# Optimization experiments

Hardware: AMD Instinct MI355X
Metric: run time of the kernel (lower is better)

## Reference

```python
import jax, jax.numpy as jnp
import numpy as np

B, H, W, DIM = 8, 32, 32, 768
HEADS = 12
HD = DIM // HEADS  # 64


def setup_inputs() -> dict:
    key = jax.random.key(0)
    ks = jax.random.split(key, 7)
    s = 0.02  # init scale to keep logits in a sane range
    return {
        "x": jax.random.normal(ks[0], (B, H, W, DIM), jnp.float32),
        "qkv_w": jax.random.normal(ks[1], (3 * DIM, DIM), jnp.float32) * s,
        "qkv_b": jax.random.normal(ks[2], (3 * DIM,), jnp.float32) * s,
        "proj_w": jax.random.normal(ks[3], (DIM, DIM), jnp.float32) * s,
        "proj_b": jax.random.normal(ks[4], (DIM,), jnp.float32) * s,
        "rel_pos_h": jax.random.normal(ks[5], (2 * H - 1, HD), jnp.float32) * s,
        "rel_pos_w": jax.random.normal(ks[6], (2 * W - 1, HD), jnp.float32) * s,
    }


def reference(x, qkv_w, qkv_b, proj_w, proj_b, rel_pos_h, rel_pos_w):
    b, h, w, dim = x.shape
    n = h * w
    hd = dim // HEADS
    scale = hd ** -0.5

    xf = x.reshape(b, n, dim)
    qkv = xf @ qkv_w.T + qkv_b                       # (B, N, 3*dim)
    qkv = qkv.reshape(b, n, 3, HEADS, hd)
    qkv = jnp.transpose(qkv, (2, 0, 3, 1, 4)).reshape(3, b * HEADS, n, hd)
    q, k, v = qkv[0], qkv[1], qkv[2]                 # each (B*heads, N, hd)

    # decomposed rel-pos bias (q_size == k_size -> pure index lookup)
    coords_h = jnp.arange(h)[:, None] - jnp.arange(h)[None, :] + (h - 1)
    coords_w = jnp.arange(w)[:, None] - jnp.arange(w)[None, :] + (w - 1)
    Rh = rel_pos_h[coords_h]                         # (H, H, hd)
    Rw = rel_pos_w[coords_w]                         # (W, W, hd)
    r_q = q.reshape(b * HEADS, h, w, hd)
    rel_h = jnp.einsum('bhwc,hkc->bhwk', r_q, Rh)    # (B*heads, H, W, H)
    rel_w = jnp.einsum('bhwc,wkc->bhwk', r_q, Rw)    # (B*heads, H, W, W)
    bias = (rel_h[:, :, :, :, None] + rel_w[:, :, :, None, :]).reshape(b * HEADS, n, n)

    attn = (q * scale) @ jnp.swapaxes(k, -2, -1) + bias
    attn = jax.nn.softmax(attn, axis=-1)
    out = attn @ v                                   # (B*heads, N, hd)

    out = out.reshape(b, HEADS, n, hd)
    out = jnp.transpose(out, (0, 2, 1, 3)).reshape(b, n, dim)
    out = out @ proj_w.T + proj_b
    return out.reshape(b, h, w, dim)
```

## Files before the change

kernel.cpp:

```cpp
#include <hip/hip_runtime.h>

typedef unsigned short u16;
typedef __attribute__((ext_vector_type(8))) short bf16x8;
typedef __attribute__((ext_vector_type(4))) short s16x4;
typedef __attribute__((ext_vector_type(4))) float f32x4;

__device__ __forceinline__ float bf2f(u16 u) {
  union { unsigned int i; float f; } v; v.i = ((unsigned int)u) << 16; return v.f;
}
__device__ __forceinline__ u16 f2bf(float f) {
  union { float f; unsigned int i; } v; v.f = f;
  unsigned int r = v.i + 0x7fffu + ((v.i >> 16) & 1u);
  return (u16)(r >> 16);
}
__device__ __forceinline__ f32x4 MFMA(bf16x8 a, bf16x8 b, f32x4 c) {
  return __builtin_amdgcn_mfma_f32_16x16x32_bf16(a, b, c, 0, 0, 0);
}
__device__ __forceinline__ void cvt8(const float* p, uint4* dst) {
  float4 f0 = *(const float4*)(p);
  float4 f1 = *(const float4*)(p + 4);
  u16* t = (u16*)dst;
  t[0] = f2bf(f0.x); t[1] = f2bf(f0.y); t[2] = f2bf(f0.z); t[3] = f2bf(f0.w);
  t[4] = f2bf(f1.x); t[5] = f2bf(f1.y); t[6] = f2bf(f1.z); t[7] = f2bf(f1.w);
}
__device__ __forceinline__ void gld16(const u16* g, u16* l) {
  __builtin_amdgcn_global_load_lds(
      (const __attribute__((address_space(1))) unsigned int*)g,
      (__attribute__((address_space(3))) unsigned int*)l, 16, 0, 0);
}

#define N8_X  786432
#define N8_QW 221184
#define N8_PW 73728
__global__ __launch_bounds__(256) void cast_kernel(
    const float* __restrict__ x, const float* __restrict__ qw, const float* __restrict__ pw,
    u16* __restrict__ xb, u16* __restrict__ qwb, u16* __restrict__ pwb)
{
  const int i = blockIdx.x * 256 + threadIdx.x;
  const float* s; u16* d; int off;
  if (i < N8_X)            { s = x;  d = xb;  off = i; }
  else if (i < N8_X+N8_QW) { s = qw; d = qwb; off = i - N8_X; }
  else                     { s = pw; d = pwb; off = i - (N8_X + N8_QW); }
  uint4 pk; cvt8(s + (size_t)off * 8, &pk);
  *(uint4*)(d + (size_t)off * 8) = pk;
}

template<int MODE>
__global__ __launch_bounds__(256) void gemm_bt(
    const u16* __restrict__ A, const u16* __restrict__ Bw, const float* __restrict__ bias,
    void* __restrict__ C0v, u16* __restrict__ C1, u16* __restrict__ C2,
    int M, int N, int K)
{
  __shared__ u16 sA[128 * 32];
  __shared__ u16 sB[128 * 32];
  const int tid = threadIdx.x;
  const int lane = tid & 63, wv = tid >> 6;
  const int wr = wv >> 1, wc = wv & 1;
  const int l16 = lane & 15, quad = lane >> 4;
  const int m0 = blockIdx.y << 7, n0 = blockIdx.x << 7;

  const int srow = tid >> 2, scol = (tid & 3) << 3;
  const u16* gA0 = A  + (size_t)(m0 + srow) * K + scol;
  const u16* gB0 = Bw + (size_t)(n0 + srow) * K + scol;
  const u16* gA1 = gA0 + (size_t)64 * K;
  const u16* gB1 = gB0 + (size_t)64 * K;
  u16* const lwA0 = sA + wv * 512;
  u16* const lwA1 = sA + 2048 + wv * 512;
  u16* const lwB0 = sB + wv * 512;
  u16* const lwB1 = sB + 2048 + wv * 512;

  f32x4 acc[4][4];
  #pragma unroll
  for (int i = 0; i < 4; ++i)
    #pragma unroll
    for (int j = 0; j < 4; ++j) {
      acc[i][j][0] = 0.f; acc[i][j][1] = 0.f; acc[i][j][2] = 0.f; acc[i][j][3] = 0.f;
    }

  for (int k0 = 0; k0 < K; k0 += 32) {
    __syncthreads();
    gld16(gA0 + k0, lwA0);
    gld16(gA1 + k0, lwA1);
    gld16(gB0 + k0, lwB0);
    gld16(gB1 + k0, lwB1);
    __syncthreads();
    bf16x8 af[4], bfr[4];
    #pragma unroll
    for (int i = 0; i < 4; ++i)
      af[i] = *(const bf16x8*)(sA + (wr * 64 + i * 16 + l16) * 32 + quad * 8);
    #pragma unroll
    for (int j = 0; j < 4; ++j)
      bfr[j] = *(const bf16x8*)(sB + (wc * 64 + j * 16 + l16) * 32 + quad * 8);
    #pragma unroll
    for (int i = 0; i < 4; ++i)
      #pragma unroll
      for (int j = 0; j < 4; ++j)
        acc[i][j] = MFMA(af[i], bfr[j], acc[i][j]);
  }

  #pragma unroll
  for (int j = 0; j < 4; ++j) {
    const int n = n0 + wc * 64 + j * 16 + l16;
    const float bv = bias[n];
    if (MODE == 0) {
      float* C0 = (float*)C0v;
      #pragma unroll
      for (int i = 0; i < 4; ++i) {
        const int m = m0 + wr * 64 + i * 16 + quad * 4;
        #pragma unroll
        for (int r = 0; r < 4; ++r)
          C0[(size_t)(m + r) * N + n] = acc[i][j][r] + bv;
      }
    } else {
      u16* C0 = (u16*)C0v;
      const int which = n / 768;
      const int rem = n - which * 768;
      const int head = rem >> 6, c = rem & 63;
      #pragma unroll
      for (int i = 0; i < 4; ++i) {
        const int m = m0 + wr * 64 + i * 16 + quad * 4;
        const int b = m >> 10, npos = m & 1023;
        const size_t bh = (size_t)(b * 12 + head);
        if (which == 0) {
          #pragma unroll
          for (int r = 0; r < 4; ++r)
            C0[(bh << 16) + ((size_t)(npos + r) << 6) + c] = f2bf(acc[i][j][r] + bv);
        } else if (which == 1) {
          #pragma unroll
          for (int r = 0; r < 4; ++r)
            C1[(bh << 16) + ((size_t)(npos + r) << 6) + c] = f2bf(acc[i][j][r] + bv);
        } else {
          s16x4 pk;
          #pragma unroll
          for (int r = 0; r < 4; ++r) pk[r] = (short)f2bf(acc[i][j][r] + bv);
          *(s16x4*)(C2 + (bh << 16) + ((size_t)c << 10) + npos) = pk;
        }
      }
    }
  }
}

__global__ __launch_bounds__(256) void attn_kernel(
    const u16* __restrict__ Q, const u16* __restrict__ Kt, const u16* __restrict__ VT,
    const float* __restrict__ rph, const float* __restrict__ rpw,
    u16* __restrict__ Oa)
{
  __shared__ __align__(16) u16 uni[18432];
  __shared__ u16 sSh[4 * 32 * 36];
  __shared__ float sL[4][32];

  u16* const uRPH = uni;
  u16* const uRPW = uni + 4536;
  u16* const uSw  = uni;
  u16* const sK   = uni;
  u16* const sVT  = uni + 4608;
  u16* const sP   = uni + 9216;

  const int tid = threadIdx.x;
  const int wave = tid >> 6, lane = tid & 63;
  const int l16 = lane & 15, quad = lane >> 4;
  const int bh = blockIdx.x >> 3, qt = blockIdx.x & 7;
  const int qrow0 = (qt << 7) + (wave << 5);
  const int qh = qrow0 >> 5;

  bf16x8 qf[2][2];
  #pragma unroll
  for (int nq = 0; nq < 2; ++nq) {
    const u16* qp = Q + (((size_t)bh << 10) + qrow0 + nq * 16 + l16) * 64 + quad * 8;
    qf[nq][0] = *(const bf16x8*)(qp);
    qf[nq][1] = *(const bf16x8*)(qp + 32);
  }

  for (int j = tid; j < 64 * 8; j += 256) {
    const int row = j >> 3, ck = (j & 7) << 3;
    uint4 vw;
    if (row < 63) cvt8(rpw + (size_t)row * 64 + ck, &vw);
    else { vw.x = 0u; vw.y = 0u; vw.z = 0u; vw.w = 0u; }
    *(uint4*)(uRPW + row * 72 + ck) = vw;
    if (row < 63) {
      uint4 vh;
      cvt8(rph + (size_t)row * 64 + ck, &vh);
      *(uint4*)(uRPH + row * 72 + ck) = vh;
    }
  }
  __syncthreads();

  #pragma unroll
  for (int tk = 0; tk < 2; ++tk) {
    const int kh = tk * 16 + l16;
    const u16* bp = uRPH + (qh + 31 - kh) * 72 + quad * 8;
    bf16x8 b0 = *(const bf16x8*)(bp);
    bf16x8 b1 = *(const bf16x8*)(bp + 32);
    #pragma unroll
    for (int nq = 0; nq < 2; ++nq) {
      f32x4 c; c[0] = 0.f; c[1] = 0.f; c[2] = 0.f; c[3] = 0.f;
      c = MFMA(qf[nq][0], b0, c);
      c = MFMA(qf[nq][1], b1, c);
      #pragma unroll
      for (int r = 0; r < 4; ++r)
        sSh[wave * 1152 + (nq * 16 + quad * 4 + r) * 36 + tk * 16 + l16] = f2bf(c[r]);
    }
  }

  f32x4 swc[2][4];
  #pragma unroll
  for (int tj = 0; tj < 4; ++tj) {
    const u16* bp = uRPW + (tj * 16 + l16) * 72 + quad * 8;
    bf16x8 b0 = *(const bf16x8*)(bp);
    bf16x8 b1 = *(const bf16x8*)(bp + 32);
    #pragma unroll
    for (int nq = 0; nq < 2; ++nq) {
      f32x4 c; c[0] = 0.f; c[1] = 0.f; c[2] = 0.f; c[3] = 0.f;
      c = MFMA(qf[nq][0], b0, c);
      c = MFMA(qf[nq][1], b1, c);
      swc[nq][tj] = c;
    }
  }
  __syncthreads();

  #pragma unroll
  for (int tj = 0; tj < 4; ++tj)
    #pragma unroll
    for (int nq = 0; nq < 2; ++nq)
      #pragma unroll
      for (int r = 0; r < 4; ++r)
        uSw[wave * 2304 + (nq * 16 + quad * 4 + r) * 72 + tj * 16 + l16] =
            f2bf(swc[nq][tj][r]);

  float rw[2][2][4];
  #pragma unroll
  for (int nq = 0; nq < 2; ++nq) {
    const int q = nq * 16 + l16;
    #pragma unroll
    for (int hi = 0; hi < 2; ++hi)
      #pragma unroll
      for (int r = 0; r < 4; ++r) {
        const int kw = hi * 16 + quad * 4 + r;
        rw[nq][hi][r] = bf2f(uSw[wave * 2304 + q * 72 + (q - kw + 31)]);
      }
  }

  f32x4 oacc[2][4];
  #pragma unroll
  for (int nq = 0; nq < 2; ++nq)
    #pragma unroll
    for (int nd = 0; nd < 4; ++nd) {
      oacc[nq][nd][0] = 0.f; oacc[nq][nd][1] = 0.f; oacc[nq][nd][2] = 0.f; oacc[nq][nd][3] = 0.f;
    }
  float lsum[2] = {0.f, 0.f};

  for (int kt = 0; kt < 16; ++kt) {
    const int kb = kt << 6;
    uint4 kreg[2], vreg[2];
    #pragma unroll
    for (int t = 0; t < 2; ++t) {
      const int j = tid + (t << 8);
      const int row = j >> 3, ck = (j & 7) << 3;
      kreg[t] = *(const uint4*)(Kt + (((size_t)bh << 10) + kb + row) * 64 + ck);
      vreg[t] = *(const uint4*)(VT + (((size_t)bh << 6) + row) * 1024 + kb + ck);
    }
    float rh[2][2];
    #pragma unroll
    for (int nq = 0; nq < 2; ++nq) {
      const unsigned int w2 =
          *(const unsigned int*)(sSh + wave * 1152 + (nq * 16 + l16) * 36 + (kt << 1));
      rh[nq][0] = bf2f((u16)(w2 & 0xffffu));
      rh[nq][1] = bf2f((u16)(w2 >> 16));
    }
    __syncthreads();
    #pragma unroll
    for (int t = 0; t < 2; ++t) {
      const int j = tid + (t << 8);
      const int row = j >> 3, ck = (j & 7) << 3;
      *(uint4*)(sK + row * 72 + ck) = kreg[t];
      *(uint4*)(sVT + row * 72 + ck) = vreg[t];
    }
    __syncthreads();

    f32x4 sacc[4][2];
    #pragma unroll
    for (int mk = 0; mk < 4; ++mk) {
      const u16* kp = sK + (mk * 16 + l16) * 72 + quad * 8;
      bf16x8 kf0 = *(const bf16x8*)(kp);
      bf16x8 kf1 = *(const bf16x8*)(kp + 32);
      #pragma unroll
      for (int nq = 0; nq < 2; ++nq) {
        f32x4 t4; t4[0] = 0.f; t4[1] = 0.f; t4[2] = 0.f; t4[3] = 0.f;
        t4 = MFMA(kf0, qf[nq][0], t4);
        t4 = MFMA(kf1, qf[nq][1], t4);
        sacc[mk][nq] = t4;
      }
    }
    #pragma unroll
    for (int nq = 0; nq < 2; ++nq) {
      #pragma unroll
      for (int mk = 0; mk < 4; ++mk) {
        const float rhv = rh[nq][mk >> 1];
        s16x4 pk;
        #pragma unroll
        for (int r = 0; r < 4; ++r) {
          const float s = sacc[mk][nq][r] * 0.125f + rhv + rw[nq][mk & 1][r];
          const float p = __expf(s);
          lsum[nq] += p;
          pk[r] = (short)f2bf(p);
        }
        *(s16x4*)(&sP[(wave << 11) + (wave << 8) + (nq * 16 + l16) * 72 + mk * 16 + quad * 4]) = pk;
      }
    }
    const u16* pw = sP + (wave << 11) + (wave << 8);
    #pragma unroll
    for (int ks = 0; ks < 2; ++ks) {
      bf16x8 ap0 = *(const bf16x8*)(pw + (l16) * 72 + ks * 32 + quad * 8);
      bf16x8 ap1 = *(const bf16x8*)(pw + (16 + l16) * 72 + ks * 32 + quad * 8);
      #pragma unroll
      for (int nd = 0; nd < 4; ++nd) {
        bf16x8 bv = *(const bf16x8*)(sVT + (nd * 16 + l16) * 72 + ks * 32 + quad * 8);
        oacc[0][nd] = MFMA(ap0, bv, oacc[0][nd]);
        oacc[1][nd] = MFMA(ap1, bv, oacc[1][nd]);
      }
    }
  }

  #pragma unroll
  for (int nq = 0; nq < 2; ++nq) {
    lsum[nq] += __shfl_xor(lsum[nq], 16);
    lsum[nq] += __shfl_xor(lsum[nq], 32);
  }
  if (lane < 16) { sL[wave][l16] = lsum[0]; sL[wave][16 + l16] = lsum[1]; }

  const int b = bh / 12, head = bh - b * 12;
  #pragma unroll
  for (int nq = 0; nq < 2; ++nq) {
    #pragma unroll
    for (int r = 0; r < 4; ++r) {
      const int ql = nq * 16 + quad * 4 + r;
      const float linv = 1.0f / sL[wave][ql];
      const size_t base = ((size_t)(b << 10) + qrow0 + ql) * 768 + head * 64 + l16;
      #pragma unroll
      for (int nd = 0; nd < 4; ++nd)
        Oa[base + nd * 16] = f2bf(oacc[nq][nd][r] * linv);
    }
  }
}

extern "C" void kernel_launch(void* const* d_in, const int* in_sizes, int n_in,
                              void* d_out, int out_size, void* d_ws, size_t ws_size,
                              hipStream_t stream) {
  (void)in_sizes; (void)n_in; (void)out_size; (void)ws_size;
  const float* x      = (const float*)d_in[0];
  const float* qkv_w  = (const float*)d_in[1];
  const float* qkv_b  = (const float*)d_in[2];
  const float* proj_w = (const float*)d_in[3];
  const float* proj_b = (const float*)d_in[4];
  const float* rph    = (const float*)d_in[5];
  const float* rpw    = (const float*)d_in[6];
  float* out = (float*)d_out;

  char* ws = (char*)d_ws;
  const size_t SZ = (size_t)96 * 1024 * 64;
  u16* Qw  = (u16*)ws;
  u16* Kw  = Qw + SZ;
  u16* VTw = Kw + SZ;
  u16* Xb  = VTw + SZ;
  u16* Oa  = Xb;
  u16* QWb = Xb + SZ;
  u16* PWb = QWb + (size_t)2304 * 768;

  cast_kernel<<<4224, 256, 0, stream>>>(x, qkv_w, proj_w, Xb, QWb, PWb);
  gemm_bt<1><<<dim3(18, 64), 256, 0, stream>>>(Xb, QWb, qkv_b, Qw, Kw, VTw, 8192, 2304, 768);
  attn_kernel<<<768, 256, 0, stream>>>(Qw, Kw, VTw, rph, rpw, Oa);
  gemm_bt<0><<<dim3(6, 64), 256, 0, stream>>>(Oa, PWb, proj_b, out, nullptr, nullptr, 8192, 768, 768);
}
```

Baseline: 251.1 us.

## Prefetch K/V tiles, remap block order, and vectorize attention output stores

The attention kernel now issues the global loads for the next K/V tile right after the shared-memory store barrier, so they overlap with the current tile's MFMA work instead of stalling at the top of each iteration. The PV MFMA operands are swapped so each lane holds four contiguous output columns, which lets the row sum stay in registers (the shared-memory sL exchange is gone) and the output be written as 8-byte vector stores. Both GEMMs and the attention kernel switch to a 1D grid with a remapped block order that groups 8 M-tiles (or 8 heads) per chunk, aiming for better L2/MALL reuse of shared operands. The cost is more live registers for the prefetch, plus one redundant reload on the last iteration.

Measured after the change: 283.5 us. 12.9% more time.

```diff
diff --git a/kernel.cpp b/kernel.cpp
--- a/kernel.cpp
+++ b/kernel.cpp
@@ -45,7 +45,7 @@
   *(uint4*)(d + (size_t)off * 8) = pk;
 }
 
-template<int MODE>
+template<int MODE, int NXB>
 __global__ __launch_bounds__(256) void gemm_bt(
     const u16* __restrict__ A, const u16* __restrict__ Bw, const float* __restrict__ bias,
     void* __restrict__ C0v, u16* __restrict__ C1, u16* __restrict__ C2,
@@ -57,7 +57,11 @@
   const int lane = tid & 63, wv = tid >> 6;
   const int wr = wv >> 1, wc = wv & 1;
   const int l16 = lane & 15, quad = lane >> 4;
-  const int m0 = blockIdx.y << 7, n0 = blockIdx.x << 7;
+  const int bi = blockIdx.x;
+  const int t = bi >> 3;
+  const int nx = t % NXB;
+  const int my = ((t / NXB) << 3) | (bi & 7);
+  const int m0 = my << 7, n0 = nx << 7;
 
   const int srow = tid >> 2, scol = (tid & 3) << 3;
   const u16* gA0 = A  + (size_t)(m0 + srow) * K + scol;
@@ -147,7 +151,6 @@
 {
   __shared__ __align__(16) u16 uni[18432];
   __shared__ u16 sSh[4 * 32 * 36];
-  __shared__ float sL[4][32];
 
   u16* const uRPH = uni;
   u16* const uRPW = uni + 4536;
@@ -159,7 +162,9 @@
   const int tid = threadIdx.x;
   const int wave = tid >> 6, lane = tid & 63;
   const int l16 = lane & 15, quad = lane >> 4;
-  const int bh = blockIdx.x >> 3, qt = blockIdx.x & 7;
+  const int bi = blockIdx.x;
+  const int bh = (bi & 7) | ((bi >> 6) << 3);
+  const int qt = (bi >> 3) & 7;
   const int qrow0 = (qt << 7) + (wave << 5);
   const int qh = qrow0 >> 5;
 
@@ -249,16 +254,19 @@
     }
   float lsum[2] = {0.f, 0.f};
 
+  uint4 kreg[2], vreg[2];
+  const int srow = tid >> 3, sck = (tid & 7) << 3;
+  const int srow2 = srow + 32;
+  #define LOADKV(ktx) do {                                                         \
+    const int kb_ = (ktx) << 6;                                                    \
+    kreg[0] = *(const uint4*)(Kt + (((size_t)bh << 10) + kb_ + srow) * 64 + sck);  \
+    vreg[0] = *(const uint4*)(VT + (((size_t)bh << 6) + srow) * 1024 + kb_ + sck); \
+    kreg[1] = *(const uint4*)(Kt + (((size_t)bh << 10) + kb_ + srow2) * 64 + sck); \
+    vreg[1] = *(const uint4*)(VT + (((size_t)bh << 6) + srow2) * 1024 + kb_ + sck);\
+  } while (0)
+
+  LOADKV(0);
   for (int kt = 0; kt < 16; ++kt) {
-    const int kb = kt << 6;
-    uint4 kreg[2], vreg[2];
-    #pragma unroll
-    for (int t = 0; t < 2; ++t) {
-      const int j = tid + (t << 8);
-      const int row = j >> 3, ck = (j & 7) << 3;
-      kreg[t] = *(const uint4*)(Kt + (((size_t)bh << 10) + kb + row) * 64 + ck);
-      vreg[t] = *(const uint4*)(VT + (((size_t)bh << 6) + row) * 1024 + kb + ck);
-    }
     float rh[2][2];
     #pragma unroll
     for (int nq = 0; nq < 2; ++nq) {
@@ -268,14 +276,13 @@
       rh[nq][1] = bf2f((u16)(w2 >> 16));
     }
     __syncthreads();
-    #pragma unroll
-    for (int t = 0; t < 2; ++t) {
-      const int j = tid + (t << 8);
-      const int row = j >> 3, ck = (j & 7) << 3;
-      *(uint4*)(sK + row * 72 + ck) = kreg[t];
-      *(uint4*)(sVT + row * 72 + ck) = vreg[t];
-    }
+    *(uint4*)(sK + srow * 72 + sck) = kreg[0];
+    *(uint4*)(sVT + srow * 72 + sck) = vreg[0];
+    *(uint4*)(sK + srow2 * 72 + sck) = kreg[1];
+    *(uint4*)(sVT + srow2 * 72 + sck) = vreg[1];
     __syncthreads();
+    const int ktn = kt < 15 ? kt + 1 : 15;
+    LOADKV(ktn);
 
     f32x4 sacc[4][2];
     #pragma unroll
@@ -315,30 +322,31 @@
       #pragma unroll
       for (int nd = 0; nd < 4; ++nd) {
         bf16x8 bv = *(const bf16x8*)(sVT + (nd * 16 + l16) * 72 + ks * 32 + quad * 8);
-        oacc[0][nd] = MFMA(ap0, bv, oacc[0][nd]);
-        oacc[1][nd] = MFMA(ap1, bv, oacc[1][nd]);
-      }
-    }
-  }
+        oacc[0][nd] = MFMA(bv, ap0, oacc[0][nd]);
+        oacc[1][nd] = MFMA(bv, ap1, oacc[1][nd]);
+      }
+    }
+  }
+  #undef LOADKV
 
   #pragma unroll
   for (int nq = 0; nq < 2; ++nq) {
     lsum[nq] += __shfl_xor(lsum[nq], 16);
     lsum[nq] += __shfl_xor(lsum[nq], 32);
   }
-  if (lane < 16) { sL[wave][l16] = lsum[0]; sL[wave][16 + l16] = lsum[1]; }
 
   const int b = bh / 12, head = bh - b * 12;
   #pragma unroll
   for (int nq = 0; nq < 2; ++nq) {
-    #pragma unroll
-    for (int r = 0; r < 4; ++r) {
-      const int ql = nq * 16 + quad * 4 + r;
-      const float linv = 1.0f / sL[wave][ql];
-      const size_t base = ((size_t)(b << 10) + qrow0 + ql) * 768 + head * 64 + l16;
-      #pragma unroll
-      for (int nd = 0; nd < 4; ++nd)
-        Oa[base + nd * 16] = f2bf(oacc[nq][nd][r] * linv);
+    const float linv = 1.0f / lsum[nq];
+    const size_t base =
+        ((size_t)(b << 10) + qrow0 + nq * 16 + l16) * 768 + head * 64 + quad * 4;
+    #pragma unroll
+    for (int nd = 0; nd < 4; ++nd) {
+      s16x4 pk;
+      #pragma unroll
+      for (int r = 0; r < 4; ++r) pk[r] = (short)f2bf(oacc[nq][nd][r] * linv);
+      *(s16x4*)(Oa + base + nd * 16) = pk;
     }
   }
 }
@@ -367,7 +375,7 @@
   u16* PWb = QWb + (size_t)2304 * 768;
 
   cast_kernel<<<4224, 256, 0, stream>>>(x, qkv_w, proj_w, Xb, QWb, PWb);
-  gemm_bt<1><<<dim3(18, 64), 256, 0, stream>>>(Xb, QWb, qkv_b, Qw, Kw, VTw, 8192, 2304, 768);
+  gemm_bt<1, 18><<<1152, 256, 0, stream>>>(Xb, QWb, qkv_b, Qw, Kw, VTw, 8192, 2304, 768);
   attn_kernel<<<768, 256, 0, stream>>>(Qw, Kw, VTw, rph, rpw, Oa);
-  gemm_bt<0><<<dim3(6, 64), 256, 0, stream>>>(Oa, PWb, proj_b, out, nullptr, nullptr, 8192, 768, 768);
-}
+  gemm_bt<0, 6><<<384, 256, 0, stream>>>(Oa, PWb, proj_b, out, nullptr, nullptr, 8192, 768, 768);
+}
```
